# Optimization experiments

Measured on AMD Instinct MI355X. Metric: run time of the kernel, lower is better.

Reference implementation:

```python
import jax, jax.numpy as jnp
import numpy as np

B, D_W, D_C, D_P = 4096, 2048, 1024, 2048
RANK = D_W // 4  # 512, per A_U/A_V shapes (d_w, d_w//4)


def setup_inputs() -> dict:
    key = jax.random.key(0)
    ks = jax.random.split(key, 10)
    return {
        "w_prev": jax.random.normal(ks[0], (B, D_W), jnp.float32),
        "z_t": jax.random.normal(ks[1], (B, D_P), jnp.float32),
        "c_t": jax.random.normal(ks[2], (B, D_C), jnp.float32),
        # params (mirroring flax init: A_diag zeros, A_U/A_V normal(0.01),
        # Dense kernels lecun_normal-ish scale, zero biases)
        "A_diag": jnp.zeros((D_W,), jnp.float32),
        "A_U": 0.01 * jax.random.normal(ks[3], (D_W, RANK), jnp.float32),
        "A_V": 0.01 * jax.random.normal(ks[4], (D_W, RANK), jnp.float32),
        "W_mod": jax.random.normal(ks[5], (D_C, D_W), jnp.float32) / np.sqrt(D_C),
        "b_mod": jnp.zeros((D_W,), jnp.float32),
        "W_B": jax.random.normal(ks[6], (D_C + D_P, D_W), jnp.float32) / np.sqrt(D_C + D_P),
        "b_B": jnp.zeros((D_W,), jnp.float32),
    }


def reference(w_prev, z_t, c_t, A_diag, A_U, A_V, W_mod, b_mod, W_B, b_B):
    # A = diag(tanh(A_diag)*0.9) + A_U @ A_V^T, row-scaled by modulation.
    # Equivalent (same math) without materializing [B, d_w, d_w]:
    #   (A * m[:, :, None]) @ w = m * (a_diag * w + A_U @ (A_V^T @ w))
    a_diag = jnp.tanh(A_diag) * 0.9                              # [d_w]
    modulation = jnp.tanh(c_t @ W_mod + b_mod)                   # [B, d_w]
    Aw = a_diag * w_prev + (w_prev @ A_V) @ A_U.T                # [B, d_w]
    Bt = jnp.concatenate([c_t, z_t], axis=-1) @ W_B + b_B        # [B, d_w]
    return modulation * Aw + Bt
```

## Files before the change

### kernel.cpp

```cpp
#include <hip/hip_runtime.h>


#define DEV __device__ __forceinline__

typedef __bf16 v8bf __attribute__((ext_vector_type(8)));
typedef __bf16 v4bf __attribute__((ext_vector_type(4)));
typedef float  v4f  __attribute__((ext_vector_type(4)));

typedef __attribute__((address_space(1))) const unsigned int* as1_cuint_ptr;
typedef __attribute__((address_space(3))) unsigned int*       as3_uint_ptr;

DEV void async16(const void* g, void* l) {
  __builtin_amdgcn_global_load_lds(
      (as1_cuint_ptr)(unsigned long long)g,
      (as3_uint_ptr)(unsigned long long)l,
      16, 0, 0);
}

DEV float tanh_fast(float x) {
  x = fminf(15.f, fmaxf(-15.f, x));
  float e = __expf(2.f * x);
  return (e - 1.f) / (e + 1.f);
}


__global__ void cvt_f32_bf16(const float* __restrict__ src,
                             __bf16* __restrict__ dst, int n) {
  int i = (blockIdx.x * 256 + threadIdx.x) * 4;
  if (i + 3 < n) {
    float4 v = *reinterpret_cast<const float4*>(src + i);
    v4bf o;
    o.x = (__bf16)v.x; o.y = (__bf16)v.y; o.z = (__bf16)v.z; o.w = (__bf16)v.w;
    *reinterpret_cast<v4bf*>(dst + i) = o;
  }
}

__global__ void transpose_cvt(const float* __restrict__ src,
                              __bf16* __restrict__ dst, int R, int C) {
  __shared__ float t[32][33];
  const int c0 = blockIdx.x * 32, r0 = blockIdx.y * 32;
  const int tx = threadIdx.x & 31, ty = threadIdx.x >> 5;
#pragma unroll
  for (int rr = 0; rr < 32; rr += 8)
    t[ty + rr][tx] = src[(size_t)(r0 + ty + rr) * C + c0 + tx];
  __syncthreads();
#pragma unroll
  for (int rr = 0; rr < 32; rr += 8)
    dst[(size_t)(c0 + ty + rr) * R + r0 + tx] = (__bf16)t[tx][ty + rr];
}

__global__ void adiag_kernel(const float* __restrict__ A_diag,
                             float* __restrict__ out, int n) {
  int i = blockIdx.x * 256 + threadIdx.x;
  if (i < n) out[i] = tanh_fast(A_diag[i]) * 0.9f;
}

__global__ __launch_bounds__(256, 2) void gemm_mt(
    const __bf16* __restrict__ A0, const __bf16* __restrict__ Bt,
    int N, int K, __bf16* __restrict__ out, const float* __restrict__ adiag) {
  __shared__ __align__(16) __bf16 As[128 * 32];
  __shared__ __align__(16) __bf16 Bs[128 * 32];

  const int tid = threadIdx.x, lane = tid & 63, wid = tid >> 6;
  const int wm = wid >> 1, wn = wid & 1, l16 = lane & 15, quad = lane >> 4;
  const int m0 = blockIdx.y * 128, n0 = blockIdx.x * 128;
  const int sg_row = lane >> 2, sg_k = (lane & 3) * 8;

  v4f acc[4][4];
#pragma unroll
  for (int i = 0; i < 4; ++i)
#pragma unroll
    for (int j = 0; j < 4; ++j) { v4f zz = {0,0,0,0}; acc[i][j] = zz; }

  for (int k0 = 0; k0 < K; k0 += 32) {
    __syncthreads();
#pragma unroll
    for (int t = 0; t < 2; ++t) {
      const int chunk = wid * 2 + t;
      const int row = chunk * 16 + sg_row;
      async16((const void*)(A0 + (size_t)(m0 + row) * K + k0 + sg_k),
              (void*)&As[chunk * 512 + lane * 8]);
      async16((const void*)(Bt + (size_t)(n0 + row) * K + k0 + sg_k),
              (void*)&Bs[chunk * 512 + lane * 8]);
    }
    __syncthreads();
    const v8bf* Ap = reinterpret_cast<const v8bf*>(As);
    const v8bf* Bp = reinterpret_cast<const v8bf*>(Bs);
    v8bf a[4], b[4];
#pragma unroll
    for (int i = 0; i < 4; ++i) a[i] = Ap[(wm * 64 + i * 16 + l16) * 4 + quad];
#pragma unroll
    for (int j = 0; j < 4; ++j) b[j] = Bp[(wn * 64 + j * 16 + l16) * 4 + quad];
#pragma unroll
    for (int i = 0; i < 4; ++i)
#pragma unroll
      for (int j = 0; j < 4; ++j)
        acc[i][j] = __builtin_amdgcn_mfma_f32_16x16x32_bf16(a[i], b[j],
                                                            acc[i][j], 0, 0, 0);
  }

  const int mBase = m0 + wm * 64 + quad * 4;
  const int nBase = n0 + wn * 64 + l16;
#pragma unroll
  for (int j = 0; j < 4; ++j) {
    const int n = nBase + j * 16;
#pragma unroll
    for (int i = 0; i < 4; ++i)
#pragma unroll
      for (int r = 0; r < 4; ++r) {
        const int m = mBase + i * 16 + r;
        float v = acc[i][j][r];
        if (m == n) v += adiag[m];
        out[(size_t)m * N + n] = (__bf16)v;
      }
  }
}

__global__ __launch_bounds__(256, 2) void fused_main(
    const __bf16* __restrict__ c, const __bf16* __restrict__ z,
    const __bf16* __restrict__ w, const __bf16* __restrict__ Wmodt,
    const __bf16* __restrict__ Mt, const __bf16* __restrict__ WBt,
    const float* __restrict__ b_mod, const float* __restrict__ b_B,
    float* __restrict__ out) {
  constexpr int DC = 1024, DW = 2048, KB = 3072;
  __shared__ __align__(16) __bf16 As[128 * 32];
  __shared__ __align__(16) __bf16 Bs[128 * 32];

  const int tid = threadIdx.x, lane = tid & 63, wid = tid >> 6;
  const int wm = wid >> 1, wn = wid & 1, l16 = lane & 15, quad = lane >> 4;
  const int m0 = blockIdx.y * 128;
  const int n0 = blockIdx.x * 128;
  const int sg_row = lane >> 2, sg_k = (lane & 3) * 8;
  const int ldsA = (wid * 2) * 512 + lane * 8;
  const int ldsA2 = (wid * 2 + 1) * 512 + lane * 8;
  const int rowA = (wid * 2) * 16 + sg_row;
  const int rowA2 = (wid * 2 + 1) * 16 + sg_row;

  v4f acc[4][4];
#pragma unroll
  for (int i = 0; i < 4; ++i)
#pragma unroll
    for (int j = 0; j < 4; ++j) { v4f zz = {0,0,0,0}; acc[i][j] = zz; }

  auto kstep = [&](const __bf16* gA, size_t lda, const __bf16* gB, size_t ldb,
                   int kA, int kB) {
    __syncthreads();
    async16((const void*)(gA + (size_t)(m0 + rowA) * lda + kA + sg_k),
            (void*)&As[ldsA]);
    async16((const void*)(gB + (size_t)(n0 + rowA) * ldb + kB + sg_k),
            (void*)&Bs[ldsA]);
    async16((const void*)(gA + (size_t)(m0 + rowA2) * lda + kA + sg_k),
            (void*)&As[ldsA2]);
    async16((const void*)(gB + (size_t)(n0 + rowA2) * ldb + kB + sg_k),
            (void*)&Bs[ldsA2]);
    __syncthreads();
    const v8bf* Ap = reinterpret_cast<const v8bf*>(As);
    const v8bf* Bp = reinterpret_cast<const v8bf*>(Bs);
    v8bf a[4], b[4];
#pragma unroll
    for (int i = 0; i < 4; ++i) a[i] = Ap[(wm * 64 + i * 16 + l16) * 4 + quad];
#pragma unroll
    for (int j = 0; j < 4; ++j) b[j] = Bp[(wn * 64 + j * 16 + l16) * 4 + quad];
#pragma unroll
    for (int i = 0; i < 4; ++i)
#pragma unroll
      for (int j = 0; j < 4; ++j)
        acc[i][j] = __builtin_amdgcn_mfma_f32_16x16x32_bf16(a[i], b[j],
                                                            acc[i][j], 0, 0, 0);
  };

  const int nBase = n0 + wn * 64 + l16;

  for (int k0 = 0; k0 < DC; k0 += 32) kstep(c, DC, Wmodt, DC, k0, k0);

  v4f mod_s[4][4];
#pragma unroll
  for (int j = 0; j < 4; ++j) {
    const float bn = b_mod[nBase + j * 16];
#pragma unroll
    for (int i = 0; i < 4; ++i) {
#pragma unroll
      for (int r = 0; r < 4; ++r)
        mod_s[i][j][r] = tanh_fast(acc[i][j][r] + bn);
      v4f zz = {0,0,0,0};
      acc[i][j] = zz;
    }
  }

  for (int k0 = 0; k0 < DW; k0 += 32) kstep(w, DW, Mt, DW, k0, k0);

#pragma unroll
  for (int i = 0; i < 4; ++i)
#pragma unroll
    for (int j = 0; j < 4; ++j) acc[i][j] *= mod_s[i][j];

  for (int k0 = 0; k0 < DC; k0 += 32) kstep(c, DC, WBt, KB, k0, k0);
  for (int k0 = DC; k0 < KB; k0 += 32) kstep(z, DW, WBt, KB, k0 - DC, k0);

  const int mBase = m0 + wm * 64 + quad * 4;
#pragma unroll
  for (int j = 0; j < 4; ++j) {
    const int n = nBase + j * 16;
    const float bn = b_B[n];
#pragma unroll
    for (int i = 0; i < 4; ++i)
#pragma unroll
      for (int r = 0; r < 4; ++r) {
        const int m = mBase + i * 16 + r;
        out[(size_t)m * DW + n] = acc[i][j][r] + bn;
      }
  }
}


extern "C" void kernel_launch(void* const* d_in, const int* in_sizes, int n_in,
                              void* d_out, int out_size, void* d_ws,
                              size_t ws_size, hipStream_t stream) {
  const float* w_prev = (const float*)d_in[0];
  const float* z_t    = (const float*)d_in[1];
  const float* c_t    = (const float*)d_in[2];
  const float* A_diag = (const float*)d_in[3];
  const float* A_U    = (const float*)d_in[4];
  const float* A_V    = (const float*)d_in[5];
  const float* W_mod  = (const float*)d_in[6];
  const float* b_mod  = (const float*)d_in[7];
  const float* W_B    = (const float*)d_in[8];
  const float* b_B    = (const float*)d_in[9];

  constexpr int Bsz = 4096, DW = 2048, DC = 1024, DP = 2048, RK = 512;
  const size_t MB = 1ull << 20;
  char* ws = (char*)d_ws;
  __bf16* w_bf  = (__bf16*)(ws + 0);
  __bf16* z_bf  = (__bf16*)(ws + 16 * MB);
  __bf16* c_bf  = (__bf16*)(ws + 32 * MB);
  __bf16* AU_bf = (__bf16*)(ws + 40 * MB);
  __bf16* AV_bf = (__bf16*)(ws + 42 * MB);
  __bf16* Wmodt = (__bf16*)(ws + 44 * MB);
  __bf16* WBt   = (__bf16*)(ws + 48 * MB);
  __bf16* Mt    = (__bf16*)(ws + 60 * MB);
  float*  adiag = (float*)(ws + 68 * MB);

  cvt_f32_bf16<<<(Bsz * DW) / 1024, 256, 0, stream>>>(w_prev, w_bf, Bsz * DW);
  cvt_f32_bf16<<<(Bsz * DP) / 1024, 256, 0, stream>>>(z_t, z_bf, Bsz * DP);
  cvt_f32_bf16<<<(Bsz * DC) / 1024, 256, 0, stream>>>(c_t, c_bf, Bsz * DC);
  cvt_f32_bf16<<<(DW * RK) / 1024, 256, 0, stream>>>(A_U, AU_bf, DW * RK);
  cvt_f32_bf16<<<(DW * RK) / 1024, 256, 0, stream>>>(A_V, AV_bf, DW * RK);
  transpose_cvt<<<dim3(DW / 32, DC / 32), 256, 0, stream>>>(W_mod, Wmodt, DC, DW);
  transpose_cvt<<<dim3(DW / 32, (DC + DP) / 32), 256, 0, stream>>>(W_B, WBt,
                                                                   DC + DP, DW);
  adiag_kernel<<<DW / 256, 256, 0, stream>>>(A_diag, adiag, DW);

  gemm_mt<<<dim3(DW / 128, DW / 128), 256, 0, stream>>>(AU_bf, AV_bf, DW, RK,
                                                        Mt, adiag);

  fused_main<<<dim3(DW / 128, Bsz / 128), 256, 0, stream>>>(
      c_bf, z_bf, w_bf, Wmodt, Mt, WBt, b_mod, b_B, (float*)d_out);
}
```

Before: 334.0 us.

## Swizzle LDS tiles, merge conversion launches, fold adiag into gemm epilogue

Applies an XOR swizzle to the k-chunk position in both the global-to-LDS async loads and the MFMA fragment reads, in both GEMM kernels, to reduce LDS bank conflicts. Merges the five fp32-to-bf16 conversion launches into one kernel and the two transpose launches into another. Drops the separate adiag kernel by computing tanh of the diagonal inline in the gemm_mt epilogue. Together these cut launch overhead and shared-memory conflicts, but add a few index operations per thread and rely on the swizzle being consistent between the load and read sides.

```diff
diff --git a/kernel.cpp b/kernel.cpp
--- a/kernel.cpp
+++ b/kernel.cpp
@@ -24,21 +24,37 @@
 }
 
 
-__global__ void cvt_f32_bf16(const float* __restrict__ src,
-                             __bf16* __restrict__ dst, int n) {
-  int i = (blockIdx.x * 256 + threadIdx.x) * 4;
-  if (i + 3 < n) {
-    float4 v = *reinterpret_cast<const float4*>(src + i);
-    v4bf o;
-    o.x = (__bf16)v.x; o.y = (__bf16)v.y; o.z = (__bf16)v.z; o.w = (__bf16)v.w;
-    *reinterpret_cast<v4bf*>(dst + i) = o;
-  }
-}
-
-__global__ void transpose_cvt(const float* __restrict__ src,
-                              __bf16* __restrict__ dst, int R, int C) {
+__global__ void cvt_all(const float* __restrict__ w, const float* __restrict__ z,
+                        const float* __restrict__ c, const float* __restrict__ au,
+                        const float* __restrict__ av,
+                        __bf16* __restrict__ wb, __bf16* __restrict__ zb,
+                        __bf16* __restrict__ cb, __bf16* __restrict__ aub,
+                        __bf16* __restrict__ avb) {
+  int b = blockIdx.x;
+  const float* src; __bf16* dst; int off;
+  if (b < 8192)        { src = w;  dst = wb;  off = b; }
+  else if (b < 16384)  { src = z;  dst = zb;  off = b - 8192; }
+  else if (b < 20480)  { src = c;  dst = cb;  off = b - 16384; }
+  else if (b < 21504)  { src = au; dst = aub; off = b - 20480; }
+  else                 { src = av; dst = avb; off = b - 21504; }
+  size_t i = (size_t)off * 1024 + (size_t)threadIdx.x * 4;
+  float4 v = *reinterpret_cast<const float4*>(src + i);
+  v4bf o;
+  o.x = (__bf16)v.x; o.y = (__bf16)v.y; o.z = (__bf16)v.z; o.w = (__bf16)v.w;
+  *reinterpret_cast<v4bf*>(dst + i) = o;
+}
+
+__global__ void transpose_both(const float* __restrict__ Wmod,
+                               const float* __restrict__ WB,
+                               __bf16* __restrict__ Wmodt,
+                               __bf16* __restrict__ WBt) {
   __shared__ float t[32][33];
-  const int c0 = blockIdx.x * 32, r0 = blockIdx.y * 32;
+  int b = blockIdx.x;
+  const float* src; __bf16* dst; int R;
+  if (b < 2048) { src = Wmod; dst = Wmodt; R = 1024; }
+  else          { b -= 2048; src = WB; dst = WBt; R = 3072; }
+  const int c0 = (b & 63) * 32, r0 = (b >> 6) * 32;
+  const int C = 2048;
   const int tx = threadIdx.x & 31, ty = threadIdx.x >> 5;
 #pragma unroll
   for (int rr = 0; rr < 32; rr += 8)
@@ -49,22 +65,18 @@
     dst[(size_t)(c0 + ty + rr) * R + r0 + tx] = (__bf16)t[tx][ty + rr];
 }
 
-__global__ void adiag_kernel(const float* __restrict__ A_diag,
-                             float* __restrict__ out, int n) {
-  int i = blockIdx.x * 256 + threadIdx.x;
-  if (i < n) out[i] = tanh_fast(A_diag[i]) * 0.9f;
-}
-
 __global__ __launch_bounds__(256, 2) void gemm_mt(
     const __bf16* __restrict__ A0, const __bf16* __restrict__ Bt,
-    int N, int K, __bf16* __restrict__ out, const float* __restrict__ adiag) {
+    int N, int K, __bf16* __restrict__ out, const float* __restrict__ A_diag) {
   __shared__ __align__(16) __bf16 As[128 * 32];
   __shared__ __align__(16) __bf16 Bs[128 * 32];
 
   const int tid = threadIdx.x, lane = tid & 63, wid = tid >> 6;
   const int wm = wid >> 1, wn = wid & 1, l16 = lane & 15, quad = lane >> 4;
   const int m0 = blockIdx.y * 128, n0 = blockIdx.x * 128;
-  const int sg_row = lane >> 2, sg_k = (lane & 3) * 8;
+  const int sg_row = lane >> 2;
+  const int sk = ((lane & 3) ^ ((lane >> 3) & 3)) * 8;
+  const int qs = quad ^ ((l16 >> 1) & 3);
 
   v4f acc[4][4];
 #pragma unroll
@@ -78,9 +90,9 @@
     for (int t = 0; t < 2; ++t) {
       const int chunk = wid * 2 + t;
       const int row = chunk * 16 + sg_row;
-      async16((const void*)(A0 + (size_t)(m0 + row) * K + k0 + sg_k),
+      async16((const void*)(A0 + (size_t)(m0 + row) * K + k0 + sk),
               (void*)&As[chunk * 512 + lane * 8]);
-      async16((const void*)(Bt + (size_t)(n0 + row) * K + k0 + sg_k),
+      async16((const void*)(Bt + (size_t)(n0 + row) * K + k0 + sk),
               (void*)&Bs[chunk * 512 + lane * 8]);
     }
     __syncthreads();
@@ -88,9 +100,9 @@
     const v8bf* Bp = reinterpret_cast<const v8bf*>(Bs);
     v8bf a[4], b[4];
 #pragma unroll
-    for (int i = 0; i < 4; ++i) a[i] = Ap[(wm * 64 + i * 16 + l16) * 4 + quad];
-#pragma unroll
-    for (int j = 0; j < 4; ++j) b[j] = Bp[(wn * 64 + j * 16 + l16) * 4 + quad];
+    for (int i = 0; i < 4; ++i) a[i] = Ap[(wm * 64 + i * 16 + l16) * 4 + qs];
+#pragma unroll
+    for (int j = 0; j < 4; ++j) b[j] = Bp[(wn * 64 + j * 16 + l16) * 4 + qs];
 #pragma unroll
     for (int i = 0; i < 4; ++i)
 #pragma unroll
@@ -110,7 +122,7 @@
       for (int r = 0; r < 4; ++r) {
         const int m = mBase + i * 16 + r;
         float v = acc[i][j][r];
-        if (m == n) v += adiag[m];
+        if (m == n) v += tanh_fast(A_diag[m]) * 0.9f;
         out[(size_t)m * N + n] = (__bf16)v;
       }
   }
@@ -130,10 +142,12 @@
   const int wm = wid >> 1, wn = wid & 1, l16 = lane & 15, quad = lane >> 4;
   const int m0 = blockIdx.y * 128;
   const int n0 = blockIdx.x * 128;
-  const int sg_row = lane >> 2, sg_k = (lane & 3) * 8;
-  const int ldsA = (wid * 2) * 512 + lane * 8;
+  const int sg_row = lane >> 2;
+  const int sk = ((lane & 3) ^ ((lane >> 3) & 3)) * 8;
+  const int qs = quad ^ ((l16 >> 1) & 3);
+  const int ldsA  = (wid * 2) * 512 + lane * 8;
   const int ldsA2 = (wid * 2 + 1) * 512 + lane * 8;
-  const int rowA = (wid * 2) * 16 + sg_row;
+  const int rowA  = (wid * 2) * 16 + sg_row;
   const int rowA2 = (wid * 2 + 1) * 16 + sg_row;
 
   v4f acc[4][4];
@@ -145,22 +159,22 @@
   auto kstep = [&](const __bf16* gA, size_t lda, const __bf16* gB, size_t ldb,
                    int kA, int kB) {
     __syncthreads();
-    async16((const void*)(gA + (size_t)(m0 + rowA) * lda + kA + sg_k),
+    async16((const void*)(gA + (size_t)(m0 + rowA) * lda + kA + sk),
             (void*)&As[ldsA]);
-    async16((const void*)(gB + (size_t)(n0 + rowA) * ldb + kB + sg_k),
+    async16((const void*)(gB + (size_t)(n0 + rowA) * ldb + kB + sk),
             (void*)&Bs[ldsA]);
-    async16((const void*)(gA + (size_t)(m0 + rowA2) * lda + kA + sg_k),
+    async16((const void*)(gA + (size_t)(m0 + rowA2) * lda + kA + sk),
             (void*)&As[ldsA2]);
-    async16((const void*)(gB + (size_t)(n0 + rowA2) * ldb + kB + sg_k),
+    async16((const void*)(gB + (size_t)(n0 + rowA2) * ldb + kB + sk),
             (void*)&Bs[ldsA2]);
     __syncthreads();
     const v8bf* Ap = reinterpret_cast<const v8bf*>(As);
     const v8bf* Bp = reinterpret_cast<const v8bf*>(Bs);
     v8bf a[4], b[4];
 #pragma unroll
-    for (int i = 0; i < 4; ++i) a[i] = Ap[(wm * 64 + i * 16 + l16) * 4 + quad];
-#pragma unroll
-    for (int j = 0; j < 4; ++j) b[j] = Bp[(wn * 64 + j * 16 + l16) * 4 + quad];
+    for (int i = 0; i < 4; ++i) a[i] = Ap[(wm * 64 + i * 16 + l16) * 4 + qs];
+#pragma unroll
+    for (int j = 0; j < 4; ++j) b[j] = Bp[(wn * 64 + j * 16 + l16) * 4 + qs];
 #pragma unroll
     for (int i = 0; i < 4; ++i)
 #pragma unroll
@@ -227,7 +241,7 @@
   const float* W_B    = (const float*)d_in[8];
   const float* b_B    = (const float*)d_in[9];
 
-  constexpr int Bsz = 4096, DW = 2048, DC = 1024, DP = 2048, RK = 512;
+  constexpr int Bsz = 4096, DW = 2048, RK = 512;
   const size_t MB = 1ull << 20;
   char* ws = (char*)d_ws;
   __bf16* w_bf  = (__bf16*)(ws + 0);
@@ -238,20 +252,13 @@
   __bf16* Wmodt = (__bf16*)(ws + 44 * MB);
   __bf16* WBt   = (__bf16*)(ws + 48 * MB);
   __bf16* Mt    = (__bf16*)(ws + 60 * MB);
-  float*  adiag = (float*)(ws + 68 * MB);
-
-  cvt_f32_bf16<<<(Bsz * DW) / 1024, 256, 0, stream>>>(w_prev, w_bf, Bsz * DW);
-  cvt_f32_bf16<<<(Bsz * DP) / 1024, 256, 0, stream>>>(z_t, z_bf, Bsz * DP);
-  cvt_f32_bf16<<<(Bsz * DC) / 1024, 256, 0, stream>>>(c_t, c_bf, Bsz * DC);
-  cvt_f32_bf16<<<(DW * RK) / 1024, 256, 0, stream>>>(A_U, AU_bf, DW * RK);
-  cvt_f32_bf16<<<(DW * RK) / 1024, 256, 0, stream>>>(A_V, AV_bf, DW * RK);
-  transpose_cvt<<<dim3(DW / 32, DC / 32), 256, 0, stream>>>(W_mod, Wmodt, DC, DW);
-  transpose_cvt<<<dim3(DW / 32, (DC + DP) / 32), 256, 0, stream>>>(W_B, WBt,
-                                                                   DC + DP, DW);
-  adiag_kernel<<<DW / 256, 256, 0, stream>>>(A_diag, adiag, DW);
+
+  cvt_all<<<22528, 256, 0, stream>>>(w_prev, z_t, c_t, A_U, A_V,
+                                     w_bf, z_bf, c_bf, AU_bf, AV_bf);
+  transpose_both<<<2048 + 6144, 256, 0, stream>>>(W_mod, W_B, Wmodt, WBt);
 
   gemm_mt<<<dim3(DW / 128, DW / 128), 256, 0, stream>>>(AU_bf, AV_bf, DW, RK,
-                                                        Mt, adiag);
+                                                        Mt, A_diag);
 
   fused_main<<<dim3(DW / 128, Bsz / 128), 256, 0, stream>>>(
       c_bf, z_bf, w_bf, Wmodt, Mt, WBt, b_mod, b_B, (float*)d_out);
```

Measured after the change: 314.3 us. 5.9% less time.
